# Kernel tuning notes

Hardware: AMD Instinct MI355X
Metric: run time of the kernel (lower is better)

Reference implementation:

```python
import jax, jax.numpy as jnp
import numpy as np

B, S, D, H = 2, 2048, 1024, 16
HEAD_DIM = D // H
MAX_REL = 64  # max_relative_position in source


def setup_inputs() -> dict:
    key = jax.random.key(0)
    ks = jax.random.split(key, 8)
    std = 0.02
    return {
        "query": jax.random.normal(ks[0], (B, S, D), jnp.float32),
        "key": jax.random.normal(ks[1], (B, S, D), jnp.float32),
        "value": jax.random.normal(ks[2], (B, S, D), jnp.float32),
        "attention_mask": jnp.zeros((B, 1, 1, S), jnp.float32),
        "Wq": jax.random.normal(ks[3], (D, D), jnp.float32) * std,
        "bq": jnp.zeros((D,), jnp.float32),
        "Wk": jax.random.normal(ks[4], (D, D), jnp.float32) * std,
        "bk": jnp.zeros((D,), jnp.float32),
        "Wv": jax.random.normal(ks[5], (D, D), jnp.float32) * std,
        "bv": jnp.zeros((D,), jnp.float32),
        "rel_table": jax.random.normal(ks[6], (2 * MAX_REL + 1, HEAD_DIM), jnp.float32) * std,
    }


def _split_heads(x, b):
    # [B,S,D] -> [B,H,S,d]
    return x.reshape(b, -1, H, HEAD_DIM).transpose(0, 2, 1, 3)


def reference(query, key, value, attention_mask, Wq, bq, Wk, bk, Wv, bv, rel_table):
    b, s, _ = query.shape
    q = _split_heads(query @ Wq + bq, b)   # [B,H,S,d]
    k = _split_heads(key @ Wk + bk, b)
    v = _split_heads(value @ Wv + bv, b)

    scores = jnp.einsum("bhqd,bhkd->bhqk", q, k)  # [B,H,S,S]

    # relative-position key bias: rel_k[q_idx, k_idx] = table[clip(k-q)+MAX_REL]
    idx = jnp.arange(s)
    dist = jnp.clip(idx[None, :] - idx[:, None], -MAX_REL, MAX_REL) + MAX_REL  # [S,S]
    rel_k = rel_table[dist]  # [S,S,d]
    scores = scores + jnp.einsum("bhqd,qkd->bhqk", q, rel_k)

    scores = scores / jnp.sqrt(jnp.asarray(HEAD_DIM, scores.dtype))
    scores = scores + attention_mask  # additive mask, broadcast [B,1,1,S]

    probs = jax.nn.softmax(scores, axis=-1)  # dropout is identity (p=0 / eval)
    ctx = jnp.einsum("bhqk,bhkd->bhqd", probs, v)
    ctx = ctx.transpose(0, 2, 1, 3).reshape(b, s, H * HEAD_DIM)
    return ctx
```

## Files before the change

kernel.cpp:

```cpp
#include <hip/hip_runtime.h>
#include <hip/hip_bf16.h>

#define BB 2
#define SS 2048
#define DD 1024
#define HH 16
#define HD 64
#define NREL 129
#define LOG2E 1.4426950408889634f
#define SCALEQ (LOG2E / 8.0f)
#define KVB 131072l

typedef short s8v __attribute__((ext_vector_type(8)));
typedef short s4v __attribute__((ext_vector_type(4)));
typedef float f4 __attribute__((ext_vector_type(4)));
typedef unsigned int u32x2 __attribute__((ext_vector_type(2)));

#define MFMA_BF16 __builtin_amdgcn_mfma_f32_16x16x32_bf16

__device__ __forceinline__ float bf2f(unsigned short u) {
  union { unsigned int i; float f; } x; x.i = ((unsigned int)u) << 16; return x.f;
}
__device__ __forceinline__ unsigned short f2bf(float f) {
  union { float f; unsigned int i; } x; x.f = f;
  unsigned int r = x.i + 0x7fffu + ((x.i >> 16) & 1u);
  return (unsigned short)(r >> 16);
}
__device__ __forceinline__ unsigned int pk2bf(float a, float b) {
  union { __hip_bfloat162 h2; unsigned int u; } c;
  c.h2 = __float22bfloat162_rn(float2{a, b});
  return c.u;
}
__device__ __forceinline__ void gl_lds16(const void* g, void* l) {
  __builtin_amdgcn_global_load_lds(
      (const __attribute__((address_space(1))) unsigned int*)g,
      (__attribute__((address_space(3))) unsigned int*)l, 16, 0, 0);
}

__device__ __forceinline__ u32x2 pl32(unsigned a, unsigned b) {
  return __builtin_amdgcn_permlane32_swap(a, b, false, false);
}
__device__ __forceinline__ u32x2 pl16(unsigned a, unsigned b) {
  return __builtin_amdgcn_permlane16_swap(a, b, false, false);
}
__device__ __forceinline__ s8v mkfrag(float p0, float p1, float p2, float p3,
                                      float p4, float p5, float p6, float p7) {
  u32x2 sa = pl32(pk2bf(p0, p1), pk2bf(p4, p5));
  u32x2 ta = pl16(sa[0], sa[1]);
  u32x2 sb = pl32(pk2bf(p2, p3), pk2bf(p6, p7));
  u32x2 tb = pl16(sb[0], sb[1]);
  unsigned fr[4] = {ta[0], tb[0], ta[1], tb[1]};
  return *(s8v*)fr;
}

__global__ __launch_bounds__(256) void cvt_x(
    const float* __restrict__ xq, const float* __restrict__ xk,
    const float* __restrict__ xv, const float* __restrict__ mask,
    unsigned short* __restrict__ xb, float* __restrict__ mkg) {
  const int z = blockIdx.y;
  const float* in = (z == 0) ? xq : (z == 1) ? xk : xv;
  unsigned short* out = xb + (long)z * 4096 * DD;
  const long i = ((long)blockIdx.x * 256 + threadIdx.x) * 8;
  f4 a = *(const f4*)(in + i);
  f4 b = *(const f4*)(in + i + 4);
  unsigned int u[4];
  u[0] = pk2bf(a[0], a[1]); u[1] = pk2bf(a[2], a[3]);
  u[2] = pk2bf(b[0], b[1]); u[3] = pk2bf(b[2], b[3]);
  *(s8v*)(out + i) = *(s8v*)u;
  if (z == 0 && blockIdx.x < BB) {
    const int row = blockIdx.x;
    const long j = (long)row * SS + threadIdx.x * 8;
    f4 ma = *(const f4*)(mask + j);
    f4 mb = *(const f4*)(mask + j + 4);
    #pragma unroll
    for (int e = 0; e < 4; ++e) {
      mkg[j + e] = ma[e] * LOG2E;
      mkg[j + 4 + e] = mb[e] * LOG2E;
    }
  }
}

__global__ __launch_bounds__(256) void cvt_w(
    const float* __restrict__ Wq, const float* __restrict__ Wk,
    const float* __restrict__ Wv, unsigned short* __restrict__ WTt) {
  __shared__ unsigned short tile[64][72];
  const int z = blockIdx.z;
  const float* in = (z == 0) ? Wq : (z == 1) ? Wk : Wv;
  unsigned short* out = WTt + (long)z * 1048576;
  const int c0 = blockIdx.x * 64, r0 = blockIdx.y * 64;
  const int t = threadIdx.x;
  const int r = t >> 2;
  #pragma unroll
  for (int j = 0; j < 4; ++j) {
    int cc = (t & 3) * 16 + j * 4;
    f4 v = *(const f4*)(in + (long)(r0 + r) * DD + c0 + cc);
    #pragma unroll
    for (int e = 0; e < 4; ++e) tile[r][cc + e] = f2bf(v[e]);
  }
  __syncthreads();
  const int c = t >> 2;
  #pragma unroll
  for (int h = 0; h < 2; ++h) {
    int r8 = (t & 3) + 4 * h;
    unsigned short vals[8];
    #pragma unroll
    for (int j = 0; j < 8; ++j) vals[j] = tile[r8 * 8 + j][c];
    int n = c0 + c, kb = r0 + r8 * 8;
    long off = ((long)(n >> 7) * 131072) + ((kb >> 6) * 8192) +
               (((kb & 63) >> 3) * 1024) + ((n & 127) * 8);
    *(s8v*)(out + off) = *(s8v*)vals;
  }
}

__global__ __launch_bounds__(256, 4) void proj_gemm(
    const unsigned short* __restrict__ Xb, const unsigned short* __restrict__ WTt,
    const float* __restrict__ bq, const float* __restrict__ bk,
    const float* __restrict__ bv,
    unsigned short* __restrict__ qbuf, unsigned short* __restrict__ ktile,
    unsigned short* __restrict__ vtile) {
  __shared__ __align__(16) unsigned short wt[8][128][8];
  unsigned short* wtf = &wt[0][0][0];
  const int z = blockIdx.z;
  const unsigned short* X = Xb + (long)z * 4096 * DD;
  const unsigned short* WTz = WTt + (long)z * 1048576;
  const float* bias = (z == 0) ? bq : (z == 1) ? bk : bv;

  const int n0 = blockIdx.x * 128, m0 = blockIdx.y * 128;
  const int t = threadIdx.x, w = t >> 6, l = t & 63;
  const int lm = l & 15, qd = l >> 4;

  f4 acc[8][2];
  #pragma unroll
  for (int i = 0; i < 8; ++i) { acc[i][0] = (f4)0.0f; acc[i][1] = (f4)0.0f; }

  const unsigned short* x0 = X + (long)(m0 + w * 32 + lm) * DD;
  const unsigned short* x1 = x0 + 16 * DD;
  const unsigned short* wtile0 = WTz + (long)(n0 >> 7) * 131072;

  for (int k0 = 0; k0 < DD; k0 += 64) {
    __syncthreads();
    const unsigned short* tb = wtile0 + (k0 >> 6) * 8192;
    #pragma unroll
    for (int i = 0; i < 4; ++i) {
      int idx = w * 4 + i;
      gl_lds16(tb + idx * 512 + l * 8, wtf + idx * 512);
    }
    s8v a00 = *(const s8v*)(x0 + k0 + qd * 8);
    s8v a01 = *(const s8v*)(x0 + k0 + 32 + qd * 8);
    s8v a10 = *(const s8v*)(x1 + k0 + qd * 8);
    s8v a11 = *(const s8v*)(x1 + k0 + 32 + qd * 8);
    asm volatile("s_waitcnt vmcnt(0)" ::: "memory");
    __syncthreads();
    #pragma unroll
    for (int cb = 0; cb < 8; ++cb) {
      s8v b0 = *(const s8v*)&wt[qd][cb * 16 + lm][0];
      s8v b1 = *(const s8v*)&wt[4 + qd][cb * 16 + lm][0];
      acc[cb][0] = MFMA_BF16(a00, b0, acc[cb][0], 0, 0, 0);
      acc[cb][0] = MFMA_BF16(a01, b1, acc[cb][0], 0, 0, 0);
      acc[cb][1] = MFMA_BF16(a10, b0, acc[cb][1], 0, 0, 0);
      acc[cb][1] = MFMA_BF16(a11, b1, acc[cb][1], 0, 0, 0);
    }
  }
  if (z == 0) {
    #pragma unroll
    for (int cb = 0; cb < 8; ++cb) {
      int n = n0 + cb * 16 + lm;
      float bvv = bias[n];
      int hh = n >> 6, d = n & 63;
      #pragma unroll
      for (int ms = 0; ms < 2; ++ms) {
        #pragma unroll
        for (int r = 0; r < 4; ++r) {
          int m = m0 + w * 32 + ms * 16 + qd * 4 + r;
          int bidx = m >> 11, s = m & (SS - 1);
          qbuf[((long)(bidx * HH + hh) * SS + s) * HD + d] =
              f2bf((acc[cb][ms][r] + bvv) * SCALEQ);
        }
      }
    }
  } else if (z == 1) {
    #pragma unroll
    for (int cb = 0; cb < 8; ++cb) {
      int n = n0 + cb * 16 + lm;
      float bvv = bias[n];
      int hh = n >> 6, d = n & 63;
      int c = d >> 3, e = d & 7;
      #pragma unroll
      for (int ms = 0; ms < 2; ++ms) {
        #pragma unroll
        for (int r = 0; r < 4; ++r) {
          int m = m0 + w * 32 + ms * 16 + qd * 4 + r;
          int bidx = m >> 11, s = m & (SS - 1);
          long bh = bidx * HH + hh;
          ktile[bh * KVB + (s >> 6) * 4096 + c * 512 + (s & 63) * 8 + e] =
              f2bf(acc[cb][ms][r] + bvv);
        }
      }
    }
  } else {
    #pragma unroll
    for (int cb = 0; cb < 8; ++cb) {
      int n = n0 + cb * 16 + lm;
      float bvv = bias[n];
      int hh = n >> 6, d = n & 63;
      #pragma unroll
      for (int ms = 0; ms < 2; ++ms) {
        int m = m0 + w * 32 + ms * 16 + qd * 4;
        int bidx = m >> 11, s = m & (SS - 1);
        long bh = bidx * HH + hh;
        unsigned short o4[4];
        #pragma unroll
        for (int r = 0; r < 4; ++r) o4[r] = f2bf(acc[cb][ms][r] + bvv);
        *(s4v*)&vtile[bh * KVB + (s >> 6) * 4096 + ((s & 63) >> 3) * 512 +
                      d * 8 + (s & 7)] = *(s4v*)o4;
      }
    }
  }
}

__global__ __launch_bounds__(256, 2) void attn(
    const unsigned short* __restrict__ qb, const unsigned short* __restrict__ ktile,
    const unsigned short* __restrict__ vtile, const float* __restrict__ tableF,
    const float* __restrict__ mkg, float* __restrict__ out) {
  __shared__ __align__(16) unsigned short ks[2][8][64][8];
  __shared__ __align__(16) unsigned short vs[2][8][64][8];
  __shared__ __align__(16) unsigned short qr2[NREL][130];

  const int bh = blockIdx.y, b = bh >> 4, h = bh & 15;
  const int q0 = blockIdx.x * 128;
  const int t = threadIdx.x, w = t >> 6, l = t & 63;
  const int lm = l & 15, qd = l >> 4;
  const int qw = q0 + w * 32;
  const int qc0 = w * 32 + lm, qc1 = qc0 + 16;

  const unsigned short* kkb = ktile + (long)bh * KVB;
  const unsigned short* vvb = vtile + (long)bh * KVB;

  #pragma unroll
  for (int i = 0; i < 2; ++i) {
    int c = 2 * w + i;
    gl_lds16(kkb + c * 512 + l * 8, &ks[0][c][0][0]);
    gl_lds16(vvb + c * 512 + l * 8, &vs[0][c][0][0]);
  }

  const unsigned short* qrow = qb + ((long)bh * SS + qw + lm) * HD;
  const s8v qa0 = *(const s8v*)(qrow + qd * 8);
  const s8v qa1 = *(const s8v*)(qrow + 32 + qd * 8);
  const s8v qb0 = *(const s8v*)(qrow + 16 * HD + qd * 8);
  const s8v qb1 = *(const s8v*)(qrow + 16 * HD + 32 + qd * 8);

  #pragma unroll
  for (int cb = 0; cb < 9; ++cb) {
    int dist = cb * 16 + lm;
    int dc = dist > NREL - 1 ? NREL - 1 : dist;
    const float* trow = tableF + dc * HD;
    f4 t0 = *(const f4*)(trow + qd * 8);
    f4 t1 = *(const f4*)(trow + qd * 8 + 4);
    f4 t2 = *(const f4*)(trow + 32 + qd * 8);
    f4 t3 = *(const f4*)(trow + 32 + qd * 8 + 4);
    unsigned int tb[8];
    tb[0] = pk2bf(t0[0], t0[1]); tb[1] = pk2bf(t0[2], t0[3]);
    tb[2] = pk2bf(t1[0], t1[1]); tb[3] = pk2bf(t1[2], t1[3]);
    tb[4] = pk2bf(t2[0], t2[1]); tb[5] = pk2bf(t2[2], t2[3]);
    tb[6] = pk2bf(t3[0], t3[1]); tb[7] = pk2bf(t3[2], t3[3]);
    s8v b0 = *(s8v*)tb, b1 = *(s8v*)(tb + 4);
    f4 c0 = MFMA_BF16(qa0, b0, (f4)0.0f, 0, 0, 0);
    c0 = MFMA_BF16(qa1, b1, c0, 0, 0, 0);
    f4 c1 = MFMA_BF16(qb0, b0, (f4)0.0f, 0, 0, 0);
    c1 = MFMA_BF16(qb1, b1, c1, 0, 0, 0);
    if (dist <= NREL - 1) {
      #pragma unroll
      for (int r = 0; r < 4; ++r) {
        qr2[dist][w * 32 + qd * 4 + r] = f2bf(c0[r]);
        qr2[dist][w * 32 + 16 + qd * 4 + r] = f2bf(c1[r]);
      }
    }
  }
  asm volatile("s_waitcnt vmcnt(0)" ::: "memory");
  __syncthreads();

  const float bLo0 = bf2f(qr2[0][qc0]), bHi0 = bf2f(qr2[128][qc0]);
  const float bLo1 = bf2f(qr2[0][qc1]), bHi1 = bf2f(qr2[128][qc1]);
  const float* mrow = mkg + b * SS;

  float m0_ = -1e30f, l0_ = 0.0f, m1_ = -1e30f, l1_ = 0.0f;
  f4 c40[4], c41[4];
  #pragma unroll
  for (int i = 0; i < 4; ++i) { c40[i] = (f4)0.0f; c41[i] = (f4)0.0f; }

  for (int rr = 0; rr < 32; ++rr) {
    const int kk = rr << 6;
    const int buf = rr & 1;
    if (rr < 31) {
      const int nb = buf ^ 1;
      const unsigned short* kg = kkb + (rr + 1) * 4096;
      const unsigned short* vg = vvb + (rr + 1) * 4096;
      #pragma unroll
      for (int i = 0; i < 2; ++i) {
        int c = 2 * w + i;
        gl_lds16(kg + c * 512 + l * 8, &ks[nb][c][0][0]);
        gl_lds16(vg + c * 512 + l * 8, &vs[nb][c][0][0]);
      }
    }
    f4 st0[4], st1[4];
    #pragma unroll
    for (int tt = 0; tt < 4; ++tt) {
      s8v k0v = *(const s8v*)&ks[buf][qd][tt * 16 + lm][0];
      s8v k1v = *(const s8v*)&ks[buf][4 + qd][tt * 16 + lm][0];
      st0[tt] = MFMA_BF16(k0v, qa0, (f4)0.0f, 0, 0, 0);
      st0[tt] = MFMA_BF16(k1v, qa1, st0[tt], 0, 0, 0);
      st1[tt] = MFMA_BF16(k0v, qb0, (f4)0.0f, 0, 0, 0);
      st1[tt] = MFMA_BF16(k1v, qb1, st1[tt], 0, 0, 0);
    }
    float z0[16], z1[16];
    const int kw = kk - qw;
    if (kw >= 96) {
      #pragma unroll
      for (int tt = 0; tt < 4; ++tt) {
        f4 mv = *(const f4*)&mrow[kk + tt * 16 + qd * 4];
        #pragma unroll
        for (int r = 0; r < 4; ++r) {
          z0[tt * 4 + r] = st0[tt][r] + bHi0 + mv[r];
          z1[tt * 4 + r] = st1[tt][r] + bHi1 + mv[r];
        }
      }
    } else if (kw <= -128) {
      #pragma unroll
      for (int tt = 0; tt < 4; ++tt) {
        f4 mv = *(const f4*)&mrow[kk + tt * 16 + qd * 4];
        #pragma unroll
        for (int r = 0; r < 4; ++r) {
          z0[tt * 4 + r] = st0[tt][r] + bLo0 + mv[r];
          z1[tt * 4 + r] = st1[tt][r] + bLo1 + mv[r];
        }
      }
    } else {
      const int db0 = kw - lm + 64 + qd * 4;
      #pragma unroll
      for (int tt = 0; tt < 4; ++tt) {
        f4 mv = *(const f4*)&mrow[kk + tt * 16 + qd * 4];
        #pragma unroll
        for (int r = 0; r < 4; ++r) {
          int du = db0 + tt * 16 + r;
          int d0 = du < 0 ? 0 : (du > 128 ? 128 : du);
          int d1 = du - 16; d1 = d1 < 0 ? 0 : (d1 > 128 ? 128 : d1);
          z0[tt * 4 + r] = st0[tt][r] + bf2f(qr2[d0][qc0]) + mv[r];
          z1[tt * 4 + r] = st1[tt][r] + bf2f(qr2[d1][qc1]) + mv[r];
        }
      }
    }
    float tm0 = z0[0], tm1 = z1[0];
    #pragma unroll
    for (int i = 1; i < 16; ++i) {
      tm0 = fmaxf(tm0, z0[i]);
      tm1 = fmaxf(tm1, z1[i]);
    }
    if (!__all(tm0 - m0_ <= 8.0f)) {
      tm0 = fmaxf(tm0, __shfl_xor(tm0, 16));
      tm0 = fmaxf(tm0, __shfl_xor(tm0, 32));
      float mn0 = fmaxf(m0_, tm0);
      float al0 = __builtin_amdgcn_exp2f(m0_ - mn0);
      m0_ = mn0; l0_ *= al0;
      #pragma unroll
      for (int db = 0; db < 4; ++db)
        #pragma unroll
        for (int r = 0; r < 4; ++r) c40[db][r] *= al0;
    }
    if (!__all(tm1 - m1_ <= 8.0f)) {
      tm1 = fmaxf(tm1, __shfl_xor(tm1, 16));
      tm1 = fmaxf(tm1, __shfl_xor(tm1, 32));
      float mn1 = fmaxf(m1_, tm1);
      float al1 = __builtin_amdgcn_exp2f(m1_ - mn1);
      m1_ = mn1; l1_ *= al1;
      #pragma unroll
      for (int db = 0; db < 4; ++db)
        #pragma unroll
        for (int r = 0; r < 4; ++r) c41[db][r] *= al1;
    }
    float s0 = 0.0f, s1 = 0.0f;
    #pragma unroll
    for (int i = 0; i < 16; ++i) {
      z0[i] = __builtin_amdgcn_exp2f(z0[i] - m0_); s0 += z0[i];
      z1[i] = __builtin_amdgcn_exp2f(z1[i] - m1_); s1 += z1[i];
    }
    s0 += __shfl_xor(s0, 16);
    s0 += __shfl_xor(s0, 32);
    s1 += __shfl_xor(s1, 16);
    s1 += __shfl_xor(s1, 32);
    l0_ += s0; l1_ += s1;

    {
      s8v pa0 = mkfrag(z0[0], z0[1], z0[2], z0[3], z0[4], z0[5], z0[6], z0[7]);
      s8v pa1 = mkfrag(z1[0], z1[1], z1[2], z1[3], z1[4], z1[5], z1[6], z1[7]);
      #pragma unroll
      for (int db = 0; db < 4; ++db) {
        s8v va = *(const s8v*)&vs[buf][qd][db * 16 + lm][0];
        c40[db] = MFMA_BF16(va, pa0, c40[db], 0, 0, 0);
        c41[db] = MFMA_BF16(va, pa1, c41[db], 0, 0, 0);
      }
    }
    {
      s8v pB0 = mkfrag(z0[8], z0[9], z0[10], z0[11], z0[12], z0[13], z0[14], z0[15]);
      s8v pB1 = mkfrag(z1[8], z1[9], z1[10], z1[11], z1[12], z1[13], z1[14], z1[15]);
      #pragma unroll
      for (int db = 0; db < 4; ++db) {
        s8v vb = *(const s8v*)&vs[buf][4 + qd][db * 16 + lm][0];
        c40[db] = MFMA_BF16(vb, pB0, c40[db], 0, 0, 0);
        c41[db] = MFMA_BF16(vb, pB1, c41[db], 0, 0, 0);
      }
    }
    asm volatile("s_waitcnt vmcnt(0)" ::: "memory");
    __syncthreads();
  }

  const float inv0 = 1.0f / l0_, inv1 = 1.0f / l1_;
  float* ob0 = out + ((long)b * SS + q0 + qc0) * DD + h * HD;
  float* ob1 = out + ((long)b * SS + q0 + qc1) * DD + h * HD;
  #pragma unroll
  for (int db = 0; db < 4; ++db) {
    f4 o0, o1;
    #pragma unroll
    for (int r = 0; r < 4; ++r) {
      o0[r] = c40[db][r] * inv0;
      o1[r] = c41[db][r] * inv1;
    }
    *(f4*)(ob0 + db * 16 + qd * 4) = o0;
    *(f4*)(ob1 + db * 16 + qd * 4) = o1;
  }
}

extern "C" void kernel_launch(void* const* d_in, const int* in_sizes, int n_in,
                              void* d_out, int out_size, void* d_ws, size_t ws_size,
                              hipStream_t stream) {
  const float* query = (const float*)d_in[0];
  const float* key   = (const float*)d_in[1];
  const float* value = (const float*)d_in[2];
  const float* mask  = (const float*)d_in[3];
  const float* Wq    = (const float*)d_in[4];
  const float* bq    = (const float*)d_in[5];
  const float* Wk    = (const float*)d_in[6];
  const float* bk    = (const float*)d_in[7];
  const float* Wv    = (const float*)d_in[8];
  const float* bv    = (const float*)d_in[9];
  const float* table = (const float*)d_in[10];

  char* ws = (char*)d_ws;
  unsigned short* WTt   = (unsigned short*)(ws);
  float*          mkg   = (float*)(ws + (7l << 20));
  unsigned short* Xb    = (unsigned short*)(ws + (8l << 20));
  unsigned short* qbuf  = (unsigned short*)(ws + (32l << 20));
  unsigned short* ktile = (unsigned short*)(ws + (40l << 20));
  unsigned short* vtile = (unsigned short*)(ws + (48l << 20));

  cvt_x<<<dim3(2048, 3, 1), 256, 0, stream>>>(query, key, value, mask, Xb, mkg);

  cvt_w<<<dim3(16, 16, 3), 256, 0, stream>>>(Wq, Wk, Wv, WTt);

  proj_gemm<<<dim3(8, 32, 3), 256, 0, stream>>>(Xb, WTt, bq, bk, bv,
                                                qbuf, ktile, vtile);

  attn<<<dim3(16, 32, 1), 256, 0, stream>>>(qbuf, ktile, vtile, table,
                                            mkg, (float*)d_out);
}
```

Baseline: 228.4 us.

## Double-buffer projection GEMM weight tiles and fuse conversion kernels into one launch

The projection GEMM now keeps two LDS buffers for weight tiles and prefetches the next K-step's weights and A fragments while MFMAs run on the current step. This is meant to hide global-load latency behind compute, and it removes one of the two barriers per iteration. The two input-conversion kernels are merged into a single launch to save launch overhead, although 1280 of the extra blocks in the fused grid exit immediately. LDS use doubles and occupancy hint drops from 4 to 2 blocks per CU, which risks lowering the number of waves resident to hide latency.

New measurement: 231.7 us. No clear change (+1.4%).

```diff
diff --git a/kernel.cpp b/kernel.cpp
--- a/kernel.cpp
+++ b/kernel.cpp
@@ -53,42 +53,45 @@
   return *(s8v*)fr;
 }
 
-__global__ __launch_bounds__(256) void cvt_x(
+__global__ __launch_bounds__(256) void cvt_fused(
     const float* __restrict__ xq, const float* __restrict__ xk,
     const float* __restrict__ xv, const float* __restrict__ mask,
-    unsigned short* __restrict__ xb, float* __restrict__ mkg) {
-  const int z = blockIdx.y;
-  const float* in = (z == 0) ? xq : (z == 1) ? xk : xv;
-  unsigned short* out = xb + (long)z * 4096 * DD;
-  const long i = ((long)blockIdx.x * 256 + threadIdx.x) * 8;
-  f4 a = *(const f4*)(in + i);
-  f4 b = *(const f4*)(in + i + 4);
-  unsigned int u[4];
-  u[0] = pk2bf(a[0], a[1]); u[1] = pk2bf(a[2], a[3]);
-  u[2] = pk2bf(b[0], b[1]); u[3] = pk2bf(b[2], b[3]);
-  *(s8v*)(out + i) = *(s8v*)u;
-  if (z == 0 && blockIdx.x < BB) {
-    const int row = blockIdx.x;
-    const long j = (long)row * SS + threadIdx.x * 8;
-    f4 ma = *(const f4*)(mask + j);
-    f4 mb = *(const f4*)(mask + j + 4);
-    #pragma unroll
-    for (int e = 0; e < 4; ++e) {
-      mkg[j + e] = ma[e] * LOG2E;
-      mkg[j + 4 + e] = mb[e] * LOG2E;
-    }
-  }
-}
-
-__global__ __launch_bounds__(256) void cvt_w(
     const float* __restrict__ Wq, const float* __restrict__ Wk,
-    const float* __restrict__ Wv, unsigned short* __restrict__ WTt) {
+    const float* __restrict__ Wv,
+    unsigned short* __restrict__ xb, float* __restrict__ mkg,
+    unsigned short* __restrict__ WTt) {
   __shared__ unsigned short tile[64][72];
-  const int z = blockIdx.z;
-  const float* in = (z == 0) ? Wq : (z == 1) ? Wk : Wv;
-  unsigned short* out = WTt + (long)z * 1048576;
-  const int c0 = blockIdx.x * 64, r0 = blockIdx.y * 64;
+  const int y = blockIdx.y;
   const int t = threadIdx.x;
+  if (y < 3) {
+    const float* in = (y == 0) ? xq : (y == 1) ? xk : xv;
+    unsigned short* out = xb + (long)y * 4096 * DD;
+    const long i = ((long)blockIdx.x * 256 + t) * 8;
+    f4 a = *(const f4*)(in + i);
+    f4 b = *(const f4*)(in + i + 4);
+    unsigned int u[4];
+    u[0] = pk2bf(a[0], a[1]); u[1] = pk2bf(a[2], a[3]);
+    u[2] = pk2bf(b[0], b[1]); u[3] = pk2bf(b[2], b[3]);
+    *(s8v*)(out + i) = *(s8v*)u;
+    if (y == 0 && blockIdx.x < BB) {
+      const int row = blockIdx.x;
+      const long j = (long)row * SS + t * 8;
+      f4 ma = *(const f4*)(mask + j);
+      f4 mb = *(const f4*)(mask + j + 4);
+      #pragma unroll
+      for (int e = 0; e < 4; ++e) {
+        mkg[j + e] = ma[e] * LOG2E;
+        mkg[j + 4 + e] = mb[e] * LOG2E;
+      }
+    }
+    return;
+  }
+  const int bx = blockIdx.x;
+  if (bx >= 768) return;
+  const int cz = bx >> 8, rem = bx & 255, cx = rem & 15, cy = rem >> 4;
+  const float* in = (cz == 0) ? Wq : (cz == 1) ? Wk : Wv;
+  unsigned short* out = WTt + (long)cz * 1048576;
+  const int c0 = cx * 64, r0 = cy * 64;
   const int r = t >> 2;
   #pragma unroll
   for (int j = 0; j < 4; ++j) {
@@ -112,14 +115,13 @@
   }
 }
 
-__global__ __launch_bounds__(256, 4) void proj_gemm(
+__global__ __launch_bounds__(256, 2) void proj_gemm(
     const unsigned short* __restrict__ Xb, const unsigned short* __restrict__ WTt,
     const float* __restrict__ bq, const float* __restrict__ bk,
     const float* __restrict__ bv,
     unsigned short* __restrict__ qbuf, unsigned short* __restrict__ ktile,
     unsigned short* __restrict__ vtile) {
-  __shared__ __align__(16) unsigned short wt[8][128][8];
-  unsigned short* wtf = &wt[0][0][0];
+  __shared__ __align__(16) unsigned short wt[2][8][128][8];
   const int z = blockIdx.z;
   const unsigned short* X = Xb + (long)z * 4096 * DD;
   const unsigned short* WTz = WTt + (long)z * 1048576;
@@ -137,30 +139,56 @@
   const unsigned short* x1 = x0 + 16 * DD;
   const unsigned short* wtile0 = WTz + (long)(n0 >> 7) * 131072;
 
-  for (int k0 = 0; k0 < DD; k0 += 64) {
-    __syncthreads();
-    const unsigned short* tb = wtile0 + (k0 >> 6) * 8192;
-    #pragma unroll
-    for (int i = 0; i < 4; ++i) {
-      int idx = w * 4 + i;
-      gl_lds16(tb + idx * 512 + l * 8, wtf + idx * 512);
-    }
-    s8v a00 = *(const s8v*)(x0 + k0 + qd * 8);
-    s8v a01 = *(const s8v*)(x0 + k0 + 32 + qd * 8);
-    s8v a10 = *(const s8v*)(x1 + k0 + qd * 8);
-    s8v a11 = *(const s8v*)(x1 + k0 + 32 + qd * 8);
+#define STAGE_WT(STEP, BUF) do {                                          \
+    const unsigned short* tb_ = wtile0 + (STEP) * 8192;                   \
+    _Pragma("unroll")                                                     \
+    for (int i_ = 0; i_ < 4; ++i_) {                                      \
+      int idx_ = w * 4 + i_;                                              \
+      gl_lds16(tb_ + idx_ * 512 + l * 8, &wt[BUF][0][0][0] + idx_ * 512); \
+    }                                                                     \
+  } while (0)
+#define LOAD_A(STEP, A) do {                                              \
+    int k0_ = (STEP) * 64;                                                \
+    A[0] = *(const s8v*)(x0 + k0_ + qd * 8);                              \
+    A[1] = *(const s8v*)(x0 + k0_ + 32 + qd * 8);                         \
+    A[2] = *(const s8v*)(x1 + k0_ + qd * 8);                              \
+    A[3] = *(const s8v*)(x1 + k0_ + 32 + qd * 8);                         \
+  } while (0)
+#define MFMA_STEP(BUF, A) do {                                            \
+    _Pragma("unroll")                                                     \
+    for (int cb_ = 0; cb_ < 8; ++cb_) {                                   \
+      s8v b0_ = *(const s8v*)&wt[BUF][qd][cb_ * 16 + lm][0];              \
+      s8v b1_ = *(const s8v*)&wt[BUF][4 + qd][cb_ * 16 + lm][0];          \
+      acc[cb_][0] = MFMA_BF16(A[0], b0_, acc[cb_][0], 0, 0, 0);           \
+      acc[cb_][0] = MFMA_BF16(A[1], b1_, acc[cb_][0], 0, 0, 0);           \
+      acc[cb_][1] = MFMA_BF16(A[2], b0_, acc[cb_][1], 0, 0, 0);           \
+      acc[cb_][1] = MFMA_BF16(A[3], b1_, acc[cb_][1], 0, 0, 0);           \
+    }                                                                     \
+  } while (0)
+
+  s8v aA[4], aB[4];
+  STAGE_WT(0, 0);
+  LOAD_A(0, aA);
+  asm volatile("s_waitcnt vmcnt(0)" ::: "memory");
+  __syncthreads();
+
+  #pragma unroll
+  for (int i = 0; i < 16; i += 2) {
+    if (i + 1 < 16) { STAGE_WT(i + 1, 1); LOAD_A(i + 1, aB); }
+    MFMA_STEP(0, aA);
     asm volatile("s_waitcnt vmcnt(0)" ::: "memory");
     __syncthreads();
-    #pragma unroll
-    for (int cb = 0; cb < 8; ++cb) {
-      s8v b0 = *(const s8v*)&wt[qd][cb * 16 + lm][0];
-      s8v b1 = *(const s8v*)&wt[4 + qd][cb * 16 + lm][0];
-      acc[cb][0] = MFMA_BF16(a00, b0, acc[cb][0], 0, 0, 0);
-      acc[cb][0] = MFMA_BF16(a01, b1, acc[cb][0], 0, 0, 0);
-      acc[cb][1] = MFMA_BF16(a10, b0, acc[cb][1], 0, 0, 0);
-      acc[cb][1] = MFMA_BF16(a11, b1, acc[cb][1], 0, 0, 0);
-    }
-  }
+    if (i + 1 < 16) {
+      if (i + 2 < 16) { STAGE_WT(i + 2, 0); LOAD_A(i + 2, aA); }
+      MFMA_STEP(1, aB);
+      asm volatile("s_waitcnt vmcnt(0)" ::: "memory");
+      __syncthreads();
+    }
+  }
+#undef STAGE_WT
+#undef LOAD_A
+#undef MFMA_STEP
+
   if (z == 0) {
     #pragma unroll
     for (int cb = 0; cb < 8; ++cb) {
@@ -452,9 +480,8 @@
   unsigned short* ktile = (unsigned short*)(ws + (40l << 20));
   unsigned short* vtile = (unsigned short*)(ws + (48l << 20));
 
-  cvt_x<<<dim3(2048, 3, 1), 256, 0, stream>>>(query, key, value, mask, Xb, mkg);
-
-  cvt_w<<<dim3(16, 16, 3), 256, 0, stream>>>(Wq, Wk, Wv, WTt);
+  cvt_fused<<<dim3(2048, 4, 1), 256, 0, stream>>>(
+      query, key, value, mask, Wq, Wk, Wv, Xb, mkg, WTt);
 
   proj_gemm<<<dim3(8, 32, 3), 256, 0, stream>>>(Xb, WTt, bq, bk, bv,
                                                 qbuf, ktile, vtile);
```
